# Kernel optimization log

Hardware: AMD Instinct MI355X
Metric: run time of the kernel (lower is better)

Reference implementation:

```python
import jax, jax.numpy as jnp
import numpy as np
from jax import lax

THRESHOLD = 0.7
OUT = 224  # output size of nn.Upsample(size=(224,224), mode='bilinear', align_corners=True)


def _bilinear(img, xs, ys):
    """align_corners=True bilinear sampling. img: (..., H, W); xs: (oh,), ys: (ow,) float coords."""
    H, W = img.shape[-2], img.shape[-1]
    x0 = jnp.clip(jnp.floor(xs).astype(jnp.int32), 0, H - 1)
    x1 = jnp.clip(x0 + 1, 0, H - 1)
    y0 = jnp.clip(jnp.floor(ys).astype(jnp.int32), 0, W - 1)
    y1 = jnp.clip(y0 + 1, 0, W - 1)
    wx = (xs - x0.astype(xs.dtype))[:, None]  # (oh,1)
    wy = (ys - y0.astype(ys.dtype))[None, :]  # (1,ow)
    top = jnp.take(img, x0, axis=-2)
    bot = jnp.take(img, x1, axis=-2)
    v00 = jnp.take(top, y0, axis=-1)
    v01 = jnp.take(top, y1, axis=-1)
    v10 = jnp.take(bot, y0, axis=-1)
    v11 = jnp.take(bot, y1, axis=-1)
    return (1 - wx) * ((1 - wy) * v00 + wy * v01) + wx * ((1 - wy) * v10 + wy * v11)


def _normalize01(h):
    n = h.shape[0]
    f = h.reshape(n, -1)
    mn = f.min(axis=1, keepdims=True)
    mx = f.max(axis=1, keepdims=True)
    return ((f - mn) / (mx - mn)).reshape(h.shape)


def _largest_cc(mask):
    """8-connected (skimage connectivity=2) largest component via min-label propagation.
    mask: (N,H,W) bool -> (N,H,W) bool, True on the largest connected component."""
    N, H, W = mask.shape
    BIG = H * W  # background sentinel label
    idx = jnp.arange(BIG, dtype=jnp.int32).reshape(1, H, W)
    lab0 = jnp.where(mask, idx, BIG)

    def body(state):
        lab, _ = state
        pooled = lax.reduce_window(lab, jnp.int32(BIG), lax.min, (1, 3, 3), (1, 1, 1), 'SAME')
        new = jnp.where(mask, pooled, BIG)
        return new, jnp.any(new != lab)

    lab, _ = lax.while_loop(lambda s: s[1], body, (lab0, jnp.bool_(True)))

    def counts(l):
        return jnp.zeros(BIG + 1, jnp.int32).at[l.reshape(-1)].add(1)

    c = jax.vmap(counts)(lab)                 # (N, H*W+1); last bin = background
    best = jnp.argmax(c[:, :BIG], axis=1)     # label of largest foreground component
    return lab == best[:, None, None]


def _bbox(lcc):
    N, H, W = lcc.shape
    rows = lcc.any(axis=2)
    cols = lcc.any(axis=1)
    has = rows.any(axis=1)
    xmin = jnp.argmax(rows, axis=1).astype(jnp.int32)
    xmax = (H - 1 - jnp.argmax(rows[:, ::-1], axis=1)).astype(jnp.int32)
    ymin = jnp.argmax(cols, axis=1).astype(jnp.int32)
    ymax = (W - 1 - jnp.argmax(cols[:, ::-1], axis=1)).astype(jnp.int32)
    # fallback to full image if the mask is empty (torch code would crash here)
    xmin = jnp.where(has, xmin, 0)
    ymin = jnp.where(has, ymin, 0)
    xmax = jnp.where(has, xmax, H - 1)
    ymax = jnp.where(has, ymax, W - 1)
    return xmin, xmax, ymin, ymax


def _crop_resize(images, xmin, xmax, ymin, ymax):
    # torch crop is images[i][:, xmin:xmax, ymin:ymax] (exclusive upper), then align_corners resize
    grid = jnp.arange(OUT, dtype=jnp.float32) / (OUT - 1)

    def one(img, a, b, c, d):
        Lx = jnp.maximum(b - a, 1)
        Ly = jnp.maximum(d - c, 1)
        xs = a.astype(jnp.float32) + grid * (Lx - 1).astype(jnp.float32)
        ys = c.astype(jnp.float32) + grid * (Ly - 1).astype(jnp.float32)
        return _bilinear(img, xs, ys)

    return jax.vmap(one)(images, xmin, xmax, ymin, ymax)


def setup_inputs() -> dict:
    key = jax.random.key(0)
    k1, k2 = jax.random.split(key)
    x = jax.random.normal(k1, (64, 3, 224, 224), dtype=jnp.float32)
    features = jax.random.normal(k2, (64, 2048, 7, 7), dtype=jnp.float32)
    return {"x": x, "features": features}


def reference(x, features):
    # distance = normalize01(Lmax(features, axis=1))
    heat = _normalize01(jnp.max(jnp.abs(features), axis=1))       # (N, h, w)
    h, w = heat.shape[1], heat.shape[2]
    grid = jnp.arange(OUT, dtype=jnp.float32) / (OUT - 1)
    out_heatmap = _bilinear(heat, grid * (h - 1), grid * (w - 1))  # (N, 224, 224)
    mask = out_heatmap > THRESHOLD
    lcc = _largest_cc(mask)
    xmin, xmax, ymin, ymax = _bbox(lcc)
    crop = _crop_resize(x, xmin, xmax, ymin, ymax)                 # (N, 3, 224, 224)
    coords = jnp.stack([ymin, xmin, ymax, xmax], axis=1)           # (N, 4), torch coord order
    return crop, out_heatmap, coords
```

## Files before the change

kernel.cpp:

```cpp
#include <hip/hip_runtime.h>
#include <stdint.h>

#define NIMG   64
#define NCH    2048
#define HW7    49
#define OUTW   224
#define NPIX   50176
#define CROP_N 9633792
#define HEAT_OFF  9633792
#define COORD_OFF 12845056
#define THRESH 0.7f

#define MAXR 8
#define RCAP (224*MAXR)
#define NWORDS 784
#define WPAD   788

#define NGRP 16

#define MASKW_BYTE_OFF 262144

__global__ __launch_bounds__(256) void k1_heat(const float* __restrict__ F,
                                               float* __restrict__ heatPart) {
    __shared__ float smax[4][64];
    const int t = threadIdx.x;
    const int b = blockIdx.x;
    const int n = b >> 4, g = b & 15;
    const int w = t >> 6, l = t & 63;
    const int lp = (l < HW7) ? l : 0;
    const float* base = F + (size_t)n * 100352 + (size_t)(g * 128 + w) * HW7 + lp;
    float vmax = 0.0f;
#pragma unroll 8
    for (int i = 0; i < 32; ++i) {
        vmax = fmaxf(vmax, fabsf(base[(size_t)i * 4 * HW7]));
    }
    smax[w][l] = vmax;
    __syncthreads();
    if (t < HW7) {
        float m = fmaxf(fmaxf(smax[0][t], smax[1][t]), fmaxf(smax[2][t], smax[3][t]));
        heatPart[b * HW7 + t] = m;
    }
}

__global__ __launch_bounds__(256) void k2_heatmap(const float* __restrict__ heatPart,
                                                  float* __restrict__ heatOut,
                                                  unsigned long long* __restrict__ maskW) {
#pragma clang fp contract(off)
    __shared__ float raw[HW7];
    __shared__ float h7[HW7];
    __shared__ float s_mn, s_mx;
    __shared__ float wT[OUTW];
    __shared__ int   i0T[OUTW];
    __shared__ int   i1T[OUTW];
    const int t = threadIdx.x;
    const int b = blockIdx.x;
    const int n = b >> 3, slice = b & 7;

    if (t < HW7) {
        float m = heatPart[(n * NGRP + 0) * HW7 + t];
#pragma unroll
        for (int g = 1; g < NGRP; ++g) m = fmaxf(m, heatPart[(n * NGRP + g) * HW7 + t]);
        raw[t] = m;
    }
    if (t < OUTW) {
        float gx = (float)t / 223.0f;
        float xs = gx * 6.0f;
        int x0 = (int)floorf(xs); x0 = min(max(x0, 0), 6);
        i0T[t] = x0;
        i1T[t] = min(x0 + 1, 6);
        wT[t]  = xs - (float)x0;
    }
    __syncthreads();
    if (t == 0) {
        float mn = raw[0], mx = raw[0];
        for (int i = 1; i < HW7; ++i) { float v = raw[i]; mn = fminf(mn, v); mx = fmaxf(mx, v); }
        s_mn = mn; s_mx = mx;
    }
    __syncthreads();
    if (t < HW7) h7[t] = (raw[t] - s_mn) / (s_mx - s_mn);
    __syncthreads();

    const int pbase = slice * 6272;
    for (int k = 0; k < 25; ++k) {
        int pl = k * 256 + t;
        if (pl < 6272) {
            int p = pbase + pl;
            int i = p / 224, j = p - i * 224;
            int x0 = i0T[i], x1 = i1T[i];
            int y0 = i0T[j], y1 = i1T[j];
            float wx = wT[i], wy = wT[j];
            float v00 = h7[x0 * 7 + y0], v01 = h7[x0 * 7 + y1];
            float v10 = h7[x1 * 7 + y0], v11 = h7[x1 * 7 + y1];
            float val = (1.0f - wx) * ((1.0f - wy) * v00 + wy * v01)
                      + wx * ((1.0f - wy) * v10 + wy * v11);
            heatOut[(size_t)n * NPIX + p] = val;
            unsigned long long bal = __ballot(val > THRESH);
            if ((t & 63) == 0) maskW[(size_t)n * WPAD + (p >> 6)] = bal;
        }
    }
}

__device__ inline unsigned uf_find(volatile unsigned* P, unsigned x) {
    while (true) {
        unsigned p = P[x];
        if (p == x) return x;
        unsigned gp = P[p];
        if (gp == p) return p;
        P[x] = gp;
        x = gp;
    }
}

__device__ inline void uf_merge(volatile unsigned* P, unsigned a, unsigned b) {
    while (true) {
        a = uf_find(P, a); b = uf_find(P, b);
        if (a == b) return;
        if (a > b) { unsigned tmp = a; a = b; b = tmp; }
        unsigned old = atomicCAS((unsigned*)&P[b], b, a);
        if (old == b) return;
        b = old;
    }
}

__global__ __launch_bounds__(256) void k3_ccl(const unsigned long long* __restrict__ maskW,
                                              float* __restrict__ coords) {
    __shared__ unsigned long long W[WPAD];
    __shared__ unsigned short runS[RCAP], runE[RCAP];
    __shared__ unsigned char nRuns[224];
    __shared__ unsigned parent[RCAP], cnt[RCAP];
    __shared__ unsigned rmin[RCAP], rmax[RCAP], cmin[RCAP], cmax[RCAP];
    __shared__ unsigned bestScore, bestRid;
    const int t = threadIdx.x;
    const int n = blockIdx.x;

    for (int i = t; i < NWORDS; i += 256) W[i] = maskW[(size_t)n * WPAD + i];
    if (t < WPAD - NWORDS) W[NWORDS + t] = 0ull;
    for (int i = t; i < RCAP; i += 256) {
        parent[i] = (unsigned)i; cnt[i] = 0u;
        rmin[i] = 0xFFFFFFFFu; rmax[i] = 0u; cmin[i] = 0xFFFFFFFFu; cmax[i] = 0u;
    }
    if (t == 0) { bestScore = 0u; bestRid = 0u; }
    __syncthreads();

    if (t < 224) {
        const int r = t;
        const int bit0 = r * 224;
        const int w0 = bit0 >> 6, sh = bit0 & 63;
        unsigned long long rb[4];
#pragma unroll
        for (int q = 0; q < 4; ++q) {
            unsigned long long lo = W[w0 + q] >> sh;
            unsigned long long hi = sh ? (W[w0 + q + 1] << (64 - sh)) : 0ull;
            rb[q] = lo | hi;
        }
        rb[3] &= 0xFFFFFFFFull;

        unsigned long long st[4], en[4];
        unsigned long long carry = 0ull;
#pragma unroll
        for (int q = 0; q < 4; ++q) {
            unsigned long long shl = (rb[q] << 1) | carry;
            carry = rb[q] >> 63;
            st[q] = rb[q] & ~shl;
        }
#pragma unroll
        for (int q = 0; q < 4; ++q) {
            unsigned long long nxt = (q < 3) ? rb[q + 1] : 0ull;
            en[q] = rb[q] & ~((rb[q] >> 1) | (nxt << 63));
        }
        int ns = 0;
#pragma unroll
        for (int q = 0; q < 4; ++q) {
            unsigned long long x = st[q];
            while (x) {
                int z = __builtin_ctzll(x); x &= x - 1;
                if (ns < MAXR) runS[r * MAXR + ns] = (unsigned short)(q * 64 + z);
                ns++;
            }
        }
        int ne = 0;
#pragma unroll
        for (int q = 0; q < 4; ++q) {
            unsigned long long x = en[q];
            while (x) {
                int z = __builtin_ctzll(x); x &= x - 1;
                if (ne < MAXR) runE[r * MAXR + ne] = (unsigned short)(q * 64 + z);
                ne++;
            }
        }
        nRuns[r] = (unsigned char)min(ns, MAXR);
    }
    __syncthreads();

    if (t >= 1 && t < 224) {
        const int r = t;
        const int na = nRuns[r], nb = nRuns[r - 1];
        for (int k = 0; k < na; ++k) {
            int rid = r * MAXR + k;
            int s = runS[rid], e = runE[rid];
            for (int m = 0; m < nb; ++m) {
                int qid = (r - 1) * MAXR + m;
                int s2 = runS[qid], e2 = runE[qid];
                if (s2 <= e + 1 && e2 >= s - 1) uf_merge(parent, (unsigned)rid, (unsigned)qid);
            }
        }
    }
    __syncthreads();

    for (int rid = t; rid < RCAP; rid += 256) {
        int r = rid >> 3, k = rid & (MAXR - 1);
        if (k < (int)nRuns[r]) {
            int s = runS[rid], e = runE[rid];
            unsigned root = uf_find(parent, (unsigned)rid);
            atomicAdd(&cnt[root], (unsigned)(e - s + 1));
            atomicMin(&rmin[root], (unsigned)r);
            atomicMax(&rmax[root], (unsigned)r);
            atomicMin(&cmin[root], (unsigned)s);
            atomicMax(&cmax[root], (unsigned)e);
        }
    }
    __syncthreads();

    for (int rid = t; rid < RCAP; rid += 256) {
        unsigned c = cnt[rid];
        if (c > 0u) {
            unsigned label = (unsigned)((rid >> 3) * 224 + (int)runS[rid]);
            unsigned score = (c << 16) | (65535u - label);
            atomicMax(&bestScore, score);
        }
    }
    __syncthreads();
    for (int rid = t; rid < RCAP; rid += 256) {
        unsigned c = cnt[rid];
        if (c > 0u) {
            unsigned label = (unsigned)((rid >> 3) * 224 + (int)runS[rid]);
            unsigned score = (c << 16) | (65535u - label);
            if (score == bestScore) bestRid = (unsigned)rid;
        }
    }
    __syncthreads();

    if (t == 0) {
        int xmin, xmax, ymin, ymax;
        if (bestScore == 0u) {
            xmin = 0; ymin = 0; xmax = 223; ymax = 223;
        } else {
            unsigned rb_ = bestRid;
            xmin = (int)rmin[rb_]; xmax = (int)rmax[rb_];
            ymin = (int)cmin[rb_]; ymax = (int)cmax[rb_];
        }
        coords[n * 4 + 0] = (float)ymin;
        coords[n * 4 + 1] = (float)xmin;
        coords[n * 4 + 2] = (float)ymax;
        coords[n * 4 + 3] = (float)xmax;
    }
}

__global__ __launch_bounds__(256) void k4_crop(const float* __restrict__ X,
                                               const float* __restrict__ coords,
                                               float* __restrict__ out) {
#pragma clang fp contract(off)
    const int t = threadIdx.x;
    const int b = blockIdx.x;
    const int n = b / 196;
    const int p = (b % 196) * 256 + t;
    const int oi = p / 224, oj = p % 224;

    int ymin = (int)coords[n * 4 + 0];
    int xmin = (int)coords[n * 4 + 1];
    int ymax = (int)coords[n * 4 + 2];
    int xmax = (int)coords[n * 4 + 3];
    int Lx = max(xmax - xmin, 1);
    int Ly = max(ymax - ymin, 1);

    float gx = (float)oi / 223.0f;
    float gy = (float)oj / 223.0f;
    float xs = (float)xmin + gx * (float)(Lx - 1);
    float ys = (float)ymin + gy * (float)(Ly - 1);
    int x0 = (int)floorf(xs); x0 = min(max(x0, 0), 223); int x1 = min(x0 + 1, 223);
    int y0 = (int)floorf(ys); y0 = min(max(y0, 0), 223); int y1 = min(y0 + 1, 223);
    float wx = xs - (float)x0;
    float wy = ys - (float)y0;

    const float* img = X + (size_t)n * 150528;
    const size_t o = (size_t)n * 150528 + (size_t)p;
    const int i00 = x0 * 224 + y0, i01 = x0 * 224 + y1;
    const int i10 = x1 * 224 + y0, i11 = x1 * 224 + y1;
#pragma unroll
    for (int ch = 0; ch < 3; ++ch) {
        const float* im = img + ch * NPIX;
        float v00 = im[i00], v01 = im[i01];
        float v10 = im[i10], v11 = im[i11];
        out[o + (size_t)ch * NPIX] =
            (1.0f - wx) * ((1.0f - wy) * v00 + wy * v01)
          + wx * ((1.0f - wy) * v10 + wy * v11);
    }
}

extern "C" void kernel_launch(void* const* d_in, const int* in_sizes, int n_in,
                              void* d_out, int out_size, void* d_ws, size_t ws_size,
                              hipStream_t stream) {
    (void)in_sizes; (void)n_in; (void)out_size; (void)d_ws; (void)ws_size;
    const float* X = (const float*)d_in[0];
    const float* F = (const float*)d_in[1];
    float* out = (float*)d_out;

    float* heatPart = (float*)d_out;
    unsigned long long* maskW = (unsigned long long*)((char*)d_out + MASKW_BYTE_OFF);
    float* heatOut = out + HEAT_OFF;
    float* coords  = out + COORD_OFF;

    k1_heat   <<<dim3(1024),  dim3(256), 0, stream>>>(F, heatPart);
    k2_heatmap<<<dim3(512),   dim3(256), 0, stream>>>(heatPart, heatOut, maskW);
    k3_ccl    <<<dim3(64),    dim3(256), 0, stream>>>(maskW, coords);
    k4_crop   <<<dim3(12544), dim3(256), 0, stream>>>(X, coords, out);
}
```

Measured before the change: 144.4 us.

## Fuse CCL into heatmap kernel via last-block counter; vectorize crop by four

The connected-component kernel is merged into the heatmap kernel. A per-image atomic counter, reset in k1, lets the last of the 8 slice blocks per image run the CCL and bounding box, which removes one launch and the gap between kernels. The crop kernel now computes four adjacent output pixels per thread and writes them as a float4, sharing row interpolation setup and cutting the block count. The fused kernel carries the large CCL shared-memory footprint in every block, which may reduce occupancy for the heatmap phase.

Result: slower. 153.1 us (+6.0%).

```diff
diff --git a/kernel.cpp b/kernel.cpp
--- a/kernel.cpp
+++ b/kernel.cpp
@@ -19,12 +19,17 @@
 #define NGRP 16
 
 #define MASKW_BYTE_OFF 262144
+#define CNT_BYTE_OFF   665600
 
 __global__ __launch_bounds__(256) void k1_heat(const float* __restrict__ F,
-                                               float* __restrict__ heatPart) {
+                                               float* __restrict__ heatPart,
+                                               unsigned* __restrict__ imgCnt) {
     __shared__ float smax[4][64];
     const int t = threadIdx.x;
     const int b = blockIdx.x;
+    if (b == 0 && t < NIMG) {
+        __hip_atomic_store(&imgCnt[t], 0u, __ATOMIC_RELAXED, __HIP_MEMORY_SCOPE_AGENT);
+    }
     const int n = b >> 4, g = b & 15;
     const int w = t >> 6, l = t & 63;
     const int lp = (l < HW7) ? l : 0;
@@ -42,9 +47,33 @@
     }
 }
 
-__global__ __launch_bounds__(256) void k2_heatmap(const float* __restrict__ heatPart,
-                                                  float* __restrict__ heatOut,
-                                                  unsigned long long* __restrict__ maskW) {
+__device__ inline unsigned uf_find(volatile unsigned* P, unsigned x) {
+    while (true) {
+        unsigned p = P[x];
+        if (p == x) return x;
+        unsigned gp = P[p];
+        if (gp == p) return p;
+        P[x] = gp;
+        x = gp;
+    }
+}
+
+__device__ inline void uf_merge(volatile unsigned* P, unsigned a, unsigned b) {
+    while (true) {
+        a = uf_find(P, a); b = uf_find(P, b);
+        if (a == b) return;
+        if (a > b) { unsigned tmp = a; a = b; b = tmp; }
+        unsigned old = atomicCAS((unsigned*)&P[b], b, a);
+        if (old == b) return;
+        b = old;
+    }
+}
+
+__global__ __launch_bounds__(256) void k2_heatmask(const float* __restrict__ heatPart,
+                                                   float* __restrict__ heatOut,
+                                                   unsigned long long* __restrict__ maskW,
+                                                   unsigned* __restrict__ imgCnt,
+                                                   float* __restrict__ coords) {
 #pragma clang fp contract(off)
     __shared__ float raw[HW7];
     __shared__ float h7[HW7];
@@ -52,6 +81,14 @@
     __shared__ float wT[OUTW];
     __shared__ int   i0T[OUTW];
     __shared__ int   i1T[OUTW];
+    __shared__ int   s_last;
+    __shared__ unsigned long long W[WPAD];
+    __shared__ unsigned short runS[RCAP], runE[RCAP];
+    __shared__ unsigned char nRuns[224];
+    __shared__ unsigned parent[RCAP], cnt[RCAP];
+    __shared__ unsigned rmin[RCAP], rmax[RCAP], cmin[RCAP], cmax[RCAP];
+    __shared__ unsigned bestScore, bestRid;
+
     const int t = threadIdx.x;
     const int b = blockIdx.x;
     const int n = b >> 3, slice = b & 7;
@@ -95,45 +132,25 @@
                       + wx * ((1.0f - wy) * v10 + wy * v11);
             heatOut[(size_t)n * NPIX + p] = val;
             unsigned long long bal = __ballot(val > THRESH);
-            if ((t & 63) == 0) maskW[(size_t)n * WPAD + (p >> 6)] = bal;
-        }
-    }
-}
-
-__device__ inline unsigned uf_find(volatile unsigned* P, unsigned x) {
-    while (true) {
-        unsigned p = P[x];
-        if (p == x) return x;
-        unsigned gp = P[p];
-        if (gp == p) return p;
-        P[x] = gp;
-        x = gp;
-    }
-}
-
-__device__ inline void uf_merge(volatile unsigned* P, unsigned a, unsigned b) {
-    while (true) {
-        a = uf_find(P, a); b = uf_find(P, b);
-        if (a == b) return;
-        if (a > b) { unsigned tmp = a; a = b; b = tmp; }
-        unsigned old = atomicCAS((unsigned*)&P[b], b, a);
-        if (old == b) return;
-        b = old;
-    }
-}
-
-__global__ __launch_bounds__(256) void k3_ccl(const unsigned long long* __restrict__ maskW,
-                                              float* __restrict__ coords) {
-    __shared__ unsigned long long W[WPAD];
-    __shared__ unsigned short runS[RCAP], runE[RCAP];
-    __shared__ unsigned char nRuns[224];
-    __shared__ unsigned parent[RCAP], cnt[RCAP];
-    __shared__ unsigned rmin[RCAP], rmax[RCAP], cmin[RCAP], cmax[RCAP];
-    __shared__ unsigned bestScore, bestRid;
-    const int t = threadIdx.x;
-    const int n = blockIdx.x;
-
-    for (int i = t; i < NWORDS; i += 256) W[i] = maskW[(size_t)n * WPAD + i];
+            if ((t & 63) == 0) {
+                __hip_atomic_store(&maskW[(size_t)n * WPAD + (p >> 6)], bal,
+                                   __ATOMIC_RELAXED, __HIP_MEMORY_SCOPE_AGENT);
+            }
+        }
+    }
+
+    __syncthreads();
+    if (t == 0) {
+        unsigned old = __hip_atomic_fetch_add(&imgCnt[n], 1u,
+                                              __ATOMIC_ACQ_REL, __HIP_MEMORY_SCOPE_AGENT);
+        s_last = (old == 7u);
+    }
+    __syncthreads();
+    if (!s_last) return;
+
+    for (int i = t; i < NWORDS; i += 256)
+        W[i] = __hip_atomic_load(&maskW[(size_t)n * WPAD + i],
+                                 __ATOMIC_RELAXED, __HIP_MEMORY_SCOPE_AGENT);
     if (t < WPAD - NWORDS) W[NWORDS + t] = 0ull;
     for (int i = t; i < RCAP; i += 256) {
         parent[i] = (unsigned)i; cnt[i] = 0u;
@@ -262,9 +279,9 @@
 #pragma clang fp contract(off)
     const int t = threadIdx.x;
     const int b = blockIdx.x;
-    const int n = b / 196;
-    const int p = (b % 196) * 256 + t;
-    const int oi = p / 224, oj = p % 224;
+    const int n = b / 49;
+    const int p4 = ((b % 49) * 256 + t) * 4;
+    const int oi = p4 / 224, oj = p4 - oi * 224;
 
     int ymin = (int)coords[n * 4 + 0];
     int xmin = (int)coords[n * 4 + 1];
@@ -274,26 +291,37 @@
     int Ly = max(ymax - ymin, 1);
 
     float gx = (float)oi / 223.0f;
-    float gy = (float)oj / 223.0f;
     float xs = (float)xmin + gx * (float)(Lx - 1);
-    float ys = (float)ymin + gy * (float)(Ly - 1);
     int x0 = (int)floorf(xs); x0 = min(max(x0, 0), 223); int x1 = min(x0 + 1, 223);
-    int y0 = (int)floorf(ys); y0 = min(max(y0, 0), 223); int y1 = min(y0 + 1, 223);
     float wx = xs - (float)x0;
-    float wy = ys - (float)y0;
+
+    int   y0q[4], y1q[4];
+    float wyq[4];
+#pragma unroll
+    for (int q = 0; q < 4; ++q) {
+        float gy = (float)(oj + q) / 223.0f;
+        float ys = (float)ymin + gy * (float)(Ly - 1);
+        int y0 = (int)floorf(ys); y0 = min(max(y0, 0), 223);
+        y0q[q] = y0; y1q[q] = min(y0 + 1, 223);
+        wyq[q] = ys - (float)y0;
+    }
 
     const float* img = X + (size_t)n * 150528;
-    const size_t o = (size_t)n * 150528 + (size_t)p;
-    const int i00 = x0 * 224 + y0, i01 = x0 * 224 + y1;
-    const int i10 = x1 * 224 + y0, i11 = x1 * 224 + y1;
+    float* obase = out + (size_t)n * 150528 + p4;
 #pragma unroll
     for (int ch = 0; ch < 3; ++ch) {
-        const float* im = img + ch * NPIX;
-        float v00 = im[i00], v01 = im[i01];
-        float v10 = im[i10], v11 = im[i11];
-        out[o + (size_t)ch * NPIX] =
-            (1.0f - wx) * ((1.0f - wy) * v00 + wy * v01)
-          + wx * ((1.0f - wy) * v10 + wy * v11);
+        const float* rt = img + ch * NPIX + x0 * 224;
+        const float* rb = img + ch * NPIX + x1 * 224;
+        float r[4];
+#pragma unroll
+        for (int q = 0; q < 4; ++q) {
+            float v00 = rt[y0q[q]], v01 = rt[y1q[q]];
+            float v10 = rb[y0q[q]], v11 = rb[y1q[q]];
+            r[q] = (1.0f - wx) * ((1.0f - wyq[q]) * v00 + wyq[q] * v01)
+                 + wx * ((1.0f - wyq[q]) * v10 + wyq[q] * v11);
+        }
+        *reinterpret_cast<float4*>(obase + (size_t)ch * NPIX) =
+            make_float4(r[0], r[1], r[2], r[3]);
     }
 }
 
@@ -307,11 +335,11 @@
 
     float* heatPart = (float*)d_out;
     unsigned long long* maskW = (unsigned long long*)((char*)d_out + MASKW_BYTE_OFF);
+    unsigned* imgCnt = (unsigned*)((char*)d_out + CNT_BYTE_OFF);
     float* heatOut = out + HEAT_OFF;
     float* coords  = out + COORD_OFF;
 
-    k1_heat   <<<dim3(1024),  dim3(256), 0, stream>>>(F, heatPart);
-    k2_heatmap<<<dim3(512),   dim3(256), 0, stream>>>(heatPart, heatOut, maskW);
-    k3_ccl    <<<dim3(64),    dim3(256), 0, stream>>>(maskW, coords);
-    k4_crop   <<<dim3(12544), dim3(256), 0, stream>>>(X, coords, out);
-}
+    k1_heat    <<<dim3(1024), dim3(256), 0, stream>>>(F, heatPart, imgCnt);
+    k2_heatmask<<<dim3(512),  dim3(256), 0, stream>>>(heatPart, heatOut, maskW, imgCnt, coords);
+    k4_crop    <<<dim3(3136), dim3(256), 0, stream>>>(X, coords, out);
+}
```
